# Kernel optimization log

Measured on AMD Instinct MI355X. Metric: run time of the kernel, lower is better.

## Reference

```python
import jax, jax.numpy as jnp
import numpy as np

H = 16
D_K = 64
HALF_WINDOW = 256  # window_size // 2 = 512 // 2


def setup_inputs() -> dict:
    key = jax.random.key(0)
    ks = jax.random.split(key, 9)
    B, S, D = 2, 2048, 1024
    scale = 0.02
    return {
        "x": jax.random.normal(ks[0], (B, S, D), dtype=jnp.float32),
        "Wq": jax.random.normal(ks[1], (D, D), dtype=jnp.float32) * scale,
        "bq": jax.random.normal(ks[2], (D,), dtype=jnp.float32) * scale,
        "Wk": jax.random.normal(ks[3], (D, D), dtype=jnp.float32) * scale,
        "bk": jax.random.normal(ks[4], (D,), dtype=jnp.float32) * scale,
        "Wv": jax.random.normal(ks[5], (D, D), dtype=jnp.float32) * scale,
        "bv": jax.random.normal(ks[6], (D,), dtype=jnp.float32) * scale,
        "Wo": jax.random.normal(ks[7], (D, D), dtype=jnp.float32) * scale,
        "bo": jax.random.normal(ks[8], (D,), dtype=jnp.float32) * scale,
    }


def reference(x, Wq, bq, Wk, bk, Wv, bv, Wo, bo):
    B, S, D = x.shape
    # projections -> [B, H, S, d_k]
    q = (x @ Wq + bq).reshape(B, S, H, D_K).transpose(0, 2, 1, 3)
    k = (x @ Wk + bk).reshape(B, S, H, D_K).transpose(0, 2, 1, 3)
    v = (x @ Wv + bv).reshape(B, S, H, D_K).transpose(0, 2, 1, 3)
    # dense scores, as in the original module
    scores = jnp.einsum("bhqd,bhkd->bhqk", q, k) / jnp.sqrt(jnp.float32(D_K))
    # sliding window band mask: 0 inside |i-j| <= half_window, -inf outside
    idx = jnp.arange(S)
    band = jnp.abs(idx[:, None] - idx[None, :]) <= HALF_WINDOW  # [S, S]
    window_mask = jnp.where(band, jnp.float32(0.0), -jnp.inf)
    scores = scores + window_mask[None, None, :, :]
    attn = jax.nn.softmax(scores, axis=-1)  # dropout is identity (p=0 / eval)
    out = jnp.einsum("bhqk,bhkd->bhqd", attn, v)  # [B, H, S, d_k]
    out = out.transpose(0, 2, 1, 3).reshape(B, S, D)
    return out @ Wo + bo
```

## Files before the change

### kernel.cpp

```cpp
#include <hip/hip_runtime.h>
#include <hip/hip_bf16.h>
#include <cstdint>
#include <cstddef>

using bf16 = __hip_bfloat16;
typedef __attribute__((ext_vector_type(8))) short bf16x8v;
typedef __attribute__((ext_vector_type(4))) float f32x4v;
typedef __attribute__((ext_vector_type(16))) float f32x16v;
typedef __attribute__((ext_vector_type(4))) int i32x4v;

__device__ __forceinline__ f32x4v mfma16x16x32(bf16x8v a, bf16x8v b, f32x4v c) {
  return __builtin_amdgcn_mfma_f32_16x16x32_bf16(a, b, c, 0, 0, 0);
}
__device__ __forceinline__ f32x16v mfma32x32x16(bf16x8v a, bf16x8v b, f32x16v c) {
  return __builtin_amdgcn_mfma_f32_32x32x16_bf16(a, b, c, 0, 0, 0);
}

__device__ __forceinline__ void lds_async16(const void* g, void* l) {
  __builtin_amdgcn_global_load_lds(
      (__attribute__((address_space(1))) void*)g,
      (__attribute__((address_space(3))) void*)l, 16, 0, 0);
}

__device__ __forceinline__ unsigned short f2bf_bits(float f) {
  union { bf16 h; unsigned short u; } cv;
  cv.h = __float2bfloat16(f);
  return cv.u;
}
__device__ __forceinline__ uint32_t pk_bf2(float a, float b) {
  return (uint32_t)f2bf_bits(a) | ((uint32_t)f2bf_bits(b) << 16);
}

#define QSC 0.18033688011111793f


__global__ void convert_x_k(const float* __restrict__ x, bf16* __restrict__ xb) {
  const int i = blockIdx.x * blockDim.x + threadIdx.x;
  const float4 v = reinterpret_cast<const float4*>(x)[i];
  ushort4 o;
  o.x = f2bf_bits(v.x); o.y = f2bf_bits(v.y);
  o.z = f2bf_bits(v.z); o.w = f2bf_bits(v.w);
  reinterpret_cast<ushort4*>(xb)[i] = o;
}

__global__ void transpose_w_k(const float* __restrict__ Wq, const float* __restrict__ Wk,
                              const float* __restrict__ Wv, const float* __restrict__ Wo,
                              bf16* __restrict__ wcat, bf16* __restrict__ wot) {
  __shared__ float tile[64][65];
  const int mat = blockIdx.z;
  const float* W = (mat == 0) ? Wq : (mat == 1) ? Wk : (mat == 2) ? Wv : Wo;
  bf16* dst = (mat < 3) ? (wcat + (size_t)mat * 1024 * 1024) : wot;
  const int n0 = blockIdx.x * 64, k0 = blockIdx.y * 64;
  const int tr = threadIdx.x >> 6, tc = threadIdx.x & 63;
#pragma unroll
  for (int it = 0; it < 16; ++it)
    tile[it * 4 + tr][tc] = W[(size_t)(k0 + it * 4 + tr) * 1024 + n0 + tc];
  __syncthreads();
#pragma unroll
  for (int it = 0; it < 16; ++it) {
    const int n = n0 + it * 4 + tr;
    dst[(size_t)n * 1024 + k0 + tc] = __float2bfloat16(tile[tc][it * 4 + tr]);
  }
}

__global__ void build_bias_k(const float* __restrict__ bq, const float* __restrict__ bk,
                             const float* __restrict__ bv, float* __restrict__ bcat) {
  const int i = blockIdx.x * 256 + threadIdx.x;
  if (i < 3072)
    bcat[i] = (i < 1024) ? bq[i] : (i < 2048) ? bk[i - 1024] : bv[i - 2048];
}

template <int EPI>
__global__ __launch_bounds__(256, 2) void gemm_k(
    const bf16* __restrict__ A, const bf16* __restrict__ Bt,
    const float* __restrict__ bias,
    bf16* __restrict__ qb, bf16* __restrict__ kb, bf16* __restrict__ vtb,
    float* __restrict__ outf)
{
  constexpr int K = 1024;
  __shared__ bf16 As[128 * 32];
  __shared__ bf16 Bs[128 * 32];
  const int t = threadIdx.x;
  const int lane = t & 63, w = t >> 6;
  const int g = lane >> 4, r = lane & 15;
  const int wr = w >> 1, wc = w & 1;
  const int m0 = blockIdx.x * 128, n0 = blockIdx.y * 128;

  const int srow = w * 16 + (lane >> 2);
  const int skoff = (lane & 3) * 8;
  const bf16* aSrc0 = A + (size_t)(m0 + srow) * K + skoff;
  const bf16* aSrc1 = aSrc0 + (size_t)64 * K;
  const bf16* bSrc0 = Bt + (size_t)(n0 + srow) * K + skoff;
  const bf16* bSrc1 = bSrc0 + (size_t)64 * K;
  bf16* aDst0 = As + w * 512;
  bf16* aDst1 = As + 2048 + w * 512;
  bf16* bDst0 = Bs + w * 512;
  bf16* bDst1 = Bs + 2048 + w * 512;

  f32x4v acc[4][4] = {};

  for (int kt = 0; kt < K; kt += 32) {
    lds_async16(aSrc0 + kt, aDst0);
    lds_async16(aSrc1 + kt, aDst1);
    lds_async16(bSrc0 + kt, bDst0);
    lds_async16(bSrc1 + kt, bDst1);
    __syncthreads();
    bf16x8v af[4], bfr[4];
#pragma unroll
    for (int m = 0; m < 4; ++m)
      af[m] = *reinterpret_cast<const bf16x8v*>(&As[(wr * 64 + m * 16 + r) * 32 + g * 8]);
#pragma unroll
    for (int n = 0; n < 4; ++n)
      bfr[n] = *reinterpret_cast<const bf16x8v*>(&Bs[(wc * 64 + n * 16 + r) * 32 + g * 8]);
#pragma unroll
    for (int m = 0; m < 4; ++m)
#pragma unroll
      for (int n = 0; n < 4; ++n)
        acc[m][n] = mfma16x16x32(af[m], bfr[n], acc[m][n]);
    __syncthreads();
  }

#pragma unroll
  for (int n = 0; n < 4; ++n) {
    const int gcol = n0 + wc * 64 + n * 16 + r;
    const float bv_ = bias[gcol];
    if (EPI == 0) {
      const int mat = gcol >> 10;
      const int d = gcol & 1023;
      const int hh = d >> 6, dk = d & 63;
#pragma unroll
      for (int m = 0; m < 4; ++m) {
#pragma unroll
        for (int v = 0; v < 4; ++v) {
          const int grow = m0 + wr * 64 + m * 16 + g * 4 + v;
          const int b = grow >> 11, s = grow & 2047;
          const float val = acc[m][n][v] + bv_;
          const size_t bh = (size_t)(b * 16 + hh);
          if (mat == 0)      qb[(bh * 2048 + s) * 64 + dk] = __float2bfloat16(val * QSC);
          else if (mat == 1) kb[(bh * 2048 + s) * 64 + dk] = __float2bfloat16(val);
          else               vtb[(bh * 64 + dk) * 2048 + s] = __float2bfloat16(val);
        }
      }
    } else {
#pragma unroll
      for (int m = 0; m < 4; ++m) {
#pragma unroll
        for (int v = 0; v < 4; ++v) {
          const int grow = m0 + wr * 64 + m * 16 + g * 4 + v;
          outf[(size_t)grow * 1024 + gcol] = acc[m][n][v] + bv_;
        }
      }
    }
  }
}

__global__ __launch_bounds__(64) void attn_k(
    const bf16* __restrict__ qb, const bf16* __restrict__ kb_,
    const bf16* __restrict__ vtb, bf16* __restrict__ aout)
{
  constexpr int S = 2048;
  const int lane = threadIdx.x & 63;
  const int hi = lane >> 5, l31 = lane & 31;
  const int d_ = blockIdx.x;
  const int xcd = d_ & 7, slot = d_ >> 3;
  const int bh_i = xcd * 4 + (slot >> 6);
  const int q0 = (slot & 63) * 32;
  const int b = bh_i >> 4, h = bh_i & 15;
  const size_t bh = (size_t)b * 16 + h;
  const bf16* qp = qb + bh * (size_t)(S * 64);
  const bf16* kp = kb_ + bh * (size_t)(S * 64);
  const bf16* vp = vtb + bh * (size_t)(64 * S);

  bf16x8v qf[4];
#pragma unroll
  for (int i = 0; i < 4; ++i)
    qf[i] = *reinterpret_cast<const bf16x8v*>(&qp[(size_t)(q0 + l31) * 64 + i * 16 + hi * 8]);

  f32x16v o0 = {}, o1 = {};
  float lrun = 0.f;

  const int jlo = (q0 >= 256) ? (q0 - 256) : 0;
  const int jend = (q0 + 256 <= S - 32) ? (q0 + 256) : (S - 32);
  const int nIter = ((jend - jlo) >> 5) + 1;

  auto LDK = [&](int j, bf16x8v* kf) {
    const bf16* p0 = kp + (size_t)(j + l31) * 64 + hi * 8;
#pragma unroll
    for (int i = 0; i < 4; ++i)
      kf[i] = *reinterpret_cast<const bf16x8v*>(p0 + i * 16);
  };
  auto LDV = [&](int j, bf16x8v* vf) {
#pragma unroll
    for (int db = 0; db < 2; ++db)
#pragma unroll
      for (int kk = 0; kk < 2; ++kk)
        vf[db * 2 + kk] = *reinterpret_cast<const bf16x8v*>(
            &vp[(size_t)(db * 32 + l31) * S + j + kk * 16 + hi * 8]);
  };

  auto STEP = [&](int idx, bf16x8v* kc, bf16x8v* vc, bf16x8v* kn, bf16x8v* vn) {
    const int j = jlo + idx * 32;
    if (idx + 1 < nIter) { LDK(j + 32, kn); LDV(j + 32, vn); }

    f32x16v s = {};
#pragma unroll
    for (int i = 0; i < 4; ++i) s = mfma32x32x16(kc[i], qf[i], s);

    float p[16];
    const bool needMask = ((q0 + 31 - j) > 256) || ((j + 31 - q0) > 256);
    if (needMask) {
      const int base = l31 - 4 * hi + (q0 - j) + 256;
#pragma unroll
      for (int t = 0; t < 4; ++t)
#pragma unroll
        for (int e = 0; e < 4; ++e) {
          const int kk_ = 8 * t + e;
          const float ev = __builtin_amdgcn_exp2f(s[4 * t + e]);
          p[4 * t + e] = ((unsigned)(base - kk_) <= 512u) ? ev : 0.f;
        }
    } else {
#pragma unroll
      for (int i = 0; i < 16; ++i) p[i] = __builtin_amdgcn_exp2f(s[i]);
    }
    lrun += (((p[0] + p[1]) + (p[2] + p[3])) + ((p[4] + p[5]) + (p[6] + p[7]))) +
            (((p[8] + p[9]) + (p[10] + p[11])) + ((p[12] + p[13]) + (p[14] + p[15])));

    uint32_t W00 = pk_bf2(p[0],  p[1]),  W01 = pk_bf2(p[2],  p[3]);
    uint32_t W10 = pk_bf2(p[4],  p[5]),  W11 = pk_bf2(p[6],  p[7]);
    uint32_t W20 = pk_bf2(p[8],  p[9]),  W21 = pk_bf2(p[10], p[11]);
    uint32_t W30 = pk_bf2(p[12], p[13]), W31 = pk_bf2(p[14], p[15]);
    asm volatile("v_permlane32_swap_b32 %0, %1" : "+v"(W00), "+v"(W10));
    asm volatile("v_permlane32_swap_b32 %0, %1" : "+v"(W01), "+v"(W11));
    asm volatile("v_permlane32_swap_b32 %0, %1" : "+v"(W20), "+v"(W30));
    asm volatile("v_permlane32_swap_b32 %0, %1" : "+v"(W21), "+v"(W31));
    union { i32x4v i; bf16x8v hv; } c0, c1;
    c0.i = (i32x4v){(int)W00, (int)W01, (int)W10, (int)W11};
    c1.i = (i32x4v){(int)W20, (int)W21, (int)W30, (int)W31};
    o0 = mfma32x32x16(vc[0], c0.hv, o0);
    o0 = mfma32x32x16(vc[1], c1.hv, o0);
    o1 = mfma32x32x16(vc[2], c0.hv, o1);
    o1 = mfma32x32x16(vc[3], c1.hv, o1);
  };

  bf16x8v ka[4], va[4], kn2[4], vn2[4];
  LDK(jlo, ka); LDV(jlo, va);
  int it = 0;
  while (it + 2 <= nIter) {
    STEP(it, ka, va, kn2, vn2);
    STEP(it + 1, kn2, vn2, ka, va);
    it += 2;
  }
  if (it < nIter) STEP(it, ka, va, kn2, vn2);

  lrun += __shfl_xor(lrun, 32);
  const float inv = 1.0f / lrun;

  const size_t ob = ((size_t)b * S + q0 + l31) * 1024 + h * 64 + hi * 4;
#pragma unroll
  for (int t = 0; t < 4; ++t) {
    uint2 u;
    u.x = pk_bf2(o0[4 * t] * inv, o0[4 * t + 1] * inv);
    u.y = pk_bf2(o0[4 * t + 2] * inv, o0[4 * t + 3] * inv);
    *reinterpret_cast<uint2*>(&aout[ob + 8 * t]) = u;
    uint2 v2;
    v2.x = pk_bf2(o1[4 * t] * inv, o1[4 * t + 1] * inv);
    v2.y = pk_bf2(o1[4 * t + 2] * inv, o1[4 * t + 3] * inv);
    *reinterpret_cast<uint2*>(&aout[ob + 32 + 8 * t]) = v2;
  }
}

extern "C" void kernel_launch(void* const* d_in, const int* in_sizes, int n_in,
                              void* d_out, int out_size, void* d_ws, size_t ws_size,
                              hipStream_t stream) {
  (void)in_sizes; (void)n_in; (void)out_size; (void)ws_size;
  const float* x  = (const float*)d_in[0];
  const float* Wq = (const float*)d_in[1];
  const float* bq = (const float*)d_in[2];
  const float* Wk = (const float*)d_in[3];
  const float* bk = (const float*)d_in[4];
  const float* Wv = (const float*)d_in[5];
  const float* bv = (const float*)d_in[6];
  const float* Wo = (const float*)d_in[7];
  const float* bo = (const float*)d_in[8];
  float* out = (float*)d_out;

  char* ws = (char*)d_ws;
  bf16*  xb    = (bf16*)(ws);
  bf16*  wcat  = (bf16*)(ws + 8388608);
  bf16*  wot   = (bf16*)(ws + 14680064);
  bf16*  qbuf  = (bf16*)(ws + 16777216);
  bf16*  kbuf  = (bf16*)(ws + 25165824);
  bf16*  vtbuf = (bf16*)(ws + 33554432);
  bf16*  aoutb = (bf16*)(ws + 41943040);
  float* bcat  = (float*)(ws + 50331648);

  convert_x_k<<<4096, 256, 0, stream>>>(x, xb);
  transpose_w_k<<<dim3(16, 16, 4), 256, 0, stream>>>(Wq, Wk, Wv, Wo, wcat, wot);
  build_bias_k<<<12, 256, 0, stream>>>(bq, bk, bv, bcat);

  gemm_k<0><<<dim3(32, 24), 256, 0, stream>>>(xb, wcat, bcat, qbuf, kbuf, vtbuf, nullptr);
  attn_k<<<2048, 64, 0, stream>>>(qbuf, kbuf, vtbuf, aoutb);
  gemm_k<1><<<dim3(32, 8), 256, 0, stream>>>(aoutb, wot, bo, nullptr, nullptr, nullptr, out);
}
```

Before: 112.4 us.

## Use 256x256-tile triple-buffered async GEMM for fused QKV projection

Replaces the 128x128 QKV projection GEMM with a dedicated kernel that uses 256x256 output tiles, 512 threads, and a three-stage LDS ring filled by async global-to-LDS loads with explicit vmcnt waits. This gives more operand reuse per tile and overlaps loads with MFMA work. It also remaps block IDs so consecutive tiles spread across XCDs. In exchange, 192 blocks is fewer than the CU count, which may leave compute units idle, and LDS use per block is larger.

```diff
diff --git a/kernel.cpp b/kernel.cpp
--- a/kernel.cpp
+++ b/kernel.cpp
@@ -70,12 +70,98 @@
     bcat[i] = (i < 1024) ? bq[i] : (i < 2048) ? bk[i - 1024] : bv[i - 2048];
 }
 
-template <int EPI>
+__global__ __launch_bounds__(512, 2) void gemm256_k(
+    const bf16* __restrict__ A, const bf16* __restrict__ Bt,
+    const float* __restrict__ bias,
+    bf16* __restrict__ qb, bf16* __restrict__ kb, bf16* __restrict__ vtb)
+{
+  constexpr int K = 1024;
+  constexpr int NTILE = 12;
+  __shared__ bf16 smem[3 * 16384];
+  const int t = threadIdx.x;
+  const int lane = t & 63, w = t >> 6;
+  const int g = lane >> 4, r = lane & 15;
+  const int wm = w >> 2, wn = w & 3;
+
+  const int d = blockIdx.x;
+  const int wg = (d & 7) * 24 + (d >> 3);
+  const int m0 = (wg / NTILE) * 256, n0 = (wg % NTILE) * 256;
+
+  const bf16* aS0 = A + (size_t)(m0 + (t >> 2)) * K + (t & 3) * 8;
+  const bf16* aS1 = aS0 + (size_t)128 * K;
+  const bf16* bS0 = Bt + (size_t)(n0 + (t >> 2)) * K + (t & 3) * 8;
+  const bf16* bS1 = bS0 + (size_t)128 * K;
+
+  f32x4v acc[8][4] = {};
+
+#define STAGE256(kt_, buf_)                                        \
+  {                                                                \
+    bf16* base_ = smem + (buf_) * 16384 + w * 512;                 \
+    const int off_ = (kt_) * 32;                                   \
+    lds_async16(aS0 + off_, base_);                                \
+    lds_async16(aS1 + off_, base_ + 4096);                         \
+    lds_async16(bS0 + off_, base_ + 8192);                         \
+    lds_async16(bS1 + off_, base_ + 12288);                        \
+  }
+
+  STAGE256(0, 0);
+  STAGE256(1, 1);
+
+  int cb = 0;
+  int sb = 2;
+  for (int kt = 0; kt < 32; ++kt) {
+    if (kt < 31) asm volatile("s_waitcnt vmcnt(4)" ::: "memory");
+    else         asm volatile("s_waitcnt vmcnt(0)" ::: "memory");
+    __builtin_amdgcn_s_barrier();
+    __builtin_amdgcn_sched_barrier(0);
+    if (kt < 30) STAGE256(kt + 2, sb);
+
+    const bf16* Ab = smem + cb * 16384 + (wm * 128 + r) * 32 + g * 8;
+    const bf16* Bb = smem + cb * 16384 + 8192 + (wn * 64 + r) * 32 + g * 8;
+    bf16x8v af[8], bfr[4];
+#pragma unroll
+    for (int m = 0; m < 8; ++m)
+      af[m] = *reinterpret_cast<const bf16x8v*>(Ab + m * 512);
+#pragma unroll
+    for (int n = 0; n < 4; ++n)
+      bfr[n] = *reinterpret_cast<const bf16x8v*>(Bb + n * 512);
+#pragma unroll
+    for (int m = 0; m < 8; ++m)
+#pragma unroll
+      for (int n = 0; n < 4; ++n)
+        acc[m][n] = mfma16x16x32(af[m], bfr[n], acc[m][n]);
+
+    cb = (cb == 2) ? 0 : cb + 1;
+    sb = (sb == 2) ? 0 : sb + 1;
+  }
+#undef STAGE256
+
+#pragma unroll
+  for (int n = 0; n < 4; ++n) {
+    const int gcol = n0 + wn * 64 + n * 16 + r;
+    const float bv_ = bias[gcol];
+    const int mat = gcol >> 10;
+    const int dcol = gcol & 1023;
+    const int hh = dcol >> 6, dk = dcol & 63;
+#pragma unroll
+    for (int m = 0; m < 8; ++m) {
+#pragma unroll
+      for (int v = 0; v < 4; ++v) {
+        const int grow = m0 + wm * 128 + m * 16 + g * 4 + v;
+        const int b = grow >> 11, s = grow & 2047;
+        const float val = acc[m][n][v] + bv_;
+        const size_t bh = (size_t)(b * 16 + hh);
+        if (mat == 0)      qb[(bh * 2048 + s) * 64 + dk] = __float2bfloat16(val * QSC);
+        else if (mat == 1) kb[(bh * 2048 + s) * 64 + dk] = __float2bfloat16(val);
+        else               vtb[(bh * 64 + dk) * 2048 + s] = __float2bfloat16(val);
+      }
+    }
+  }
+}
+
 __global__ __launch_bounds__(256, 2) void gemm_k(
     const bf16* __restrict__ A, const bf16* __restrict__ Bt,
-    const float* __restrict__ bias,
-    bf16* __restrict__ qb, bf16* __restrict__ kb, bf16* __restrict__ vtb,
-    float* __restrict__ outf)
+    const float* __restrict__ bias, float* __restrict__ outf)
 {
   constexpr int K = 1024;
   __shared__ bf16 As[128 * 32];
@@ -124,31 +210,12 @@
   for (int n = 0; n < 4; ++n) {
     const int gcol = n0 + wc * 64 + n * 16 + r;
     const float bv_ = bias[gcol];
-    if (EPI == 0) {
-      const int mat = gcol >> 10;
-      const int d = gcol & 1023;
-      const int hh = d >> 6, dk = d & 63;
-#pragma unroll
-      for (int m = 0; m < 4; ++m) {
-#pragma unroll
-        for (int v = 0; v < 4; ++v) {
-          const int grow = m0 + wr * 64 + m * 16 + g * 4 + v;
-          const int b = grow >> 11, s = grow & 2047;
-          const float val = acc[m][n][v] + bv_;
-          const size_t bh = (size_t)(b * 16 + hh);
-          if (mat == 0)      qb[(bh * 2048 + s) * 64 + dk] = __float2bfloat16(val * QSC);
-          else if (mat == 1) kb[(bh * 2048 + s) * 64 + dk] = __float2bfloat16(val);
-          else               vtb[(bh * 64 + dk) * 2048 + s] = __float2bfloat16(val);
-        }
-      }
-    } else {
-#pragma unroll
-      for (int m = 0; m < 4; ++m) {
-#pragma unroll
-        for (int v = 0; v < 4; ++v) {
-          const int grow = m0 + wr * 64 + m * 16 + g * 4 + v;
-          outf[(size_t)grow * 1024 + gcol] = acc[m][n][v] + bv_;
-        }
+#pragma unroll
+    for (int m = 0; m < 4; ++m) {
+#pragma unroll
+      for (int v = 0; v < 4; ++v) {
+        const int grow = m0 + wr * 64 + m * 16 + g * 4 + v;
+        outf[(size_t)grow * 1024 + gcol] = acc[m][n][v] + bv_;
       }
     }
   }
@@ -211,12 +278,12 @@
     if (needMask) {
       const int base = l31 - 4 * hi + (q0 - j) + 256;
 #pragma unroll
-      for (int t = 0; t < 4; ++t)
+      for (int tt = 0; tt < 4; ++tt)
 #pragma unroll
         for (int e = 0; e < 4; ++e) {
-          const int kk_ = 8 * t + e;
-          const float ev = __builtin_amdgcn_exp2f(s[4 * t + e]);
-          p[4 * t + e] = ((unsigned)(base - kk_) <= 512u) ? ev : 0.f;
+          const int kk_ = 8 * tt + e;
+          const float ev = __builtin_amdgcn_exp2f(s[4 * tt + e]);
+          p[4 * tt + e] = ((unsigned)(base - kk_) <= 512u) ? ev : 0.f;
         }
     } else {
 #pragma unroll
@@ -257,15 +324,15 @@
 
   const size_t ob = ((size_t)b * S + q0 + l31) * 1024 + h * 64 + hi * 4;
 #pragma unroll
-  for (int t = 0; t < 4; ++t) {
+  for (int tt = 0; tt < 4; ++tt) {
     uint2 u;
-    u.x = pk_bf2(o0[4 * t] * inv, o0[4 * t + 1] * inv);
-    u.y = pk_bf2(o0[4 * t + 2] * inv, o0[4 * t + 3] * inv);
-    *reinterpret_cast<uint2*>(&aout[ob + 8 * t]) = u;
+    u.x = pk_bf2(o0[4 * tt] * inv, o0[4 * tt + 1] * inv);
+    u.y = pk_bf2(o0[4 * tt + 2] * inv, o0[4 * tt + 3] * inv);
+    *reinterpret_cast<uint2*>(&aout[ob + 8 * tt]) = u;
     uint2 v2;
-    v2.x = pk_bf2(o1[4 * t] * inv, o1[4 * t + 1] * inv);
-    v2.y = pk_bf2(o1[4 * t + 2] * inv, o1[4 * t + 3] * inv);
-    *reinterpret_cast<uint2*>(&aout[ob + 32 + 8 * t]) = v2;
+    v2.x = pk_bf2(o1[4 * tt] * inv, o1[4 * tt + 1] * inv);
+    v2.y = pk_bf2(o1[4 * tt + 2] * inv, o1[4 * tt + 3] * inv);
+    *reinterpret_cast<uint2*>(&aout[ob + 32 + 8 * tt]) = v2;
   }
 }
 
@@ -298,7 +365,7 @@
   transpose_w_k<<<dim3(16, 16, 4), 256, 0, stream>>>(Wq, Wk, Wv, Wo, wcat, wot);
   build_bias_k<<<12, 256, 0, stream>>>(bq, bk, bv, bcat);
 
-  gemm_k<0><<<dim3(32, 24), 256, 0, stream>>>(xb, wcat, bcat, qbuf, kbuf, vtbuf, nullptr);
+  gemm256_k<<<192, 512, 0, stream>>>(xb, wcat, bcat, qbuf, kbuf, vtbuf);
   attn_k<<<2048, 64, 0, stream>>>(qbuf, kbuf, vtbuf, aoutb);
-  gemm_k<1><<<dim3(32, 8), 256, 0, stream>>>(aoutb, wot, bo, nullptr, nullptr, nullptr, out);
-}
+  gemm_k<<<dim3(32, 8), 256, 0, stream>>>(aoutb, wot, bo, out);
+}
```

Result: slower. 133.3 us (+18.7%).

## Deepen GEMM K-tile to 64 with XOR-swizzled LDS layout

Applied to the files above, without the earlier changes.

The projection GEMM now stages 64-wide K slices per iteration instead of 32, which halves the number of barrier pairs. Global-to-LDS loads use an XOR swizzle on the 16-byte chunk index so the fragment reads avoid LDS bank conflicts. The launch-bounds occupancy hint goes from 2 to 3 blocks, at the cost of doubled shared memory per block (32 KB) and tighter register pressure. Loop variables in the attention kernel are renamed to avoid shadowing.

```diff
diff --git a/kernel.cpp b/kernel.cpp
--- a/kernel.cpp
+++ b/kernel.cpp
@@ -71,52 +71,64 @@
 }
 
 template <int EPI>
-__global__ __launch_bounds__(256, 2) void gemm_k(
+__global__ __launch_bounds__(256, 3) void gemm_k(
     const bf16* __restrict__ A, const bf16* __restrict__ Bt,
     const float* __restrict__ bias,
     bf16* __restrict__ qb, bf16* __restrict__ kb, bf16* __restrict__ vtb,
     float* __restrict__ outf)
 {
   constexpr int K = 1024;
-  __shared__ bf16 As[128 * 32];
-  __shared__ bf16 Bs[128 * 32];
+  __shared__ bf16 As[128 * 64];
+  __shared__ bf16 Bs[128 * 64];
   const int t = threadIdx.x;
   const int lane = t & 63, w = t >> 6;
   const int g = lane >> 4, r = lane & 15;
   const int wr = w >> 1, wc = w & 1;
   const int m0 = blockIdx.x * 128, n0 = blockIdx.y * 128;
 
-  const int srow = w * 16 + (lane >> 2);
-  const int skoff = (lane & 3) * 8;
-  const bf16* aSrc0 = A + (size_t)(m0 + srow) * K + skoff;
-  const bf16* aSrc1 = aSrc0 + (size_t)64 * K;
-  const bf16* bSrc0 = Bt + (size_t)(n0 + srow) * K + skoff;
-  const bf16* bSrc1 = bSrc0 + (size_t)64 * K;
-  bf16* aDst0 = As + w * 512;
-  bf16* aDst1 = As + 2048 + w * 512;
-  bf16* bDst0 = Bs + w * 512;
-  bf16* bDst1 = Bs + 2048 + w * 512;
+  const bf16* aS[4];
+  const bf16* bS[4];
+  bf16* aD[4];
+  bf16* bD[4];
+#pragma unroll
+  for (int i = 0; i < 4; ++i) {
+    const int G = t + 256 * i;
+    const int row = G >> 3, gd = G & 7;
+    const int col = ((gd ^ (row & 7)) << 3);
+    aS[i] = A + (size_t)(m0 + row) * K + col;
+    bS[i] = Bt + (size_t)(n0 + row) * K + col;
+    aD[i] = As + w * 512 + i * 2048;
+    bD[i] = Bs + w * 512 + i * 2048;
+  }
 
   f32x4v acc[4][4] = {};
 
-  for (int kt = 0; kt < K; kt += 32) {
-    lds_async16(aSrc0 + kt, aDst0);
-    lds_async16(aSrc1 + kt, aDst1);
-    lds_async16(bSrc0 + kt, bDst0);
-    lds_async16(bSrc1 + kt, bDst1);
+  for (int kt = 0; kt < 16; ++kt) {
+    const int ko = kt * 64;
+#pragma unroll
+    for (int i = 0; i < 4; ++i) {
+      lds_async16(aS[i] + ko, aD[i]);
+      lds_async16(bS[i] + ko, bD[i]);
+    }
     __syncthreads();
-    bf16x8v af[4], bfr[4];
-#pragma unroll
-    for (int m = 0; m < 4; ++m)
-      af[m] = *reinterpret_cast<const bf16x8v*>(&As[(wr * 64 + m * 16 + r) * 32 + g * 8]);
-#pragma unroll
-    for (int n = 0; n < 4; ++n)
-      bfr[n] = *reinterpret_cast<const bf16x8v*>(&Bs[(wc * 64 + n * 16 + r) * 32 + g * 8]);
-#pragma unroll
-    for (int m = 0; m < 4; ++m)
-#pragma unroll
-      for (int n = 0; n < 4; ++n)
-        acc[m][n] = mfma16x16x32(af[m], bfr[n], acc[m][n]);
+
+#pragma unroll
+    for (int ks = 0; ks < 2; ++ks) {
+      const int csw = ((ks * 4 + g) ^ (r & 7)) << 4;
+      bf16x8v af[4];
+#pragma unroll
+      for (int m = 0; m < 4; ++m)
+        af[m] = *reinterpret_cast<const bf16x8v*>(
+            (const char*)As + (wr * 64 + m * 16 + r) * 128 + csw);
+#pragma unroll
+      for (int n = 0; n < 4; ++n) {
+        const bf16x8v bf_ = *reinterpret_cast<const bf16x8v*>(
+            (const char*)Bs + (wc * 64 + n * 16 + r) * 128 + csw);
+#pragma unroll
+        for (int m = 0; m < 4; ++m)
+          acc[m][n] = mfma16x16x32(af[m], bf_, acc[m][n]);
+      }
+    }
     __syncthreads();
   }
 
@@ -211,12 +223,12 @@
     if (needMask) {
       const int base = l31 - 4 * hi + (q0 - j) + 256;
 #pragma unroll
-      for (int t = 0; t < 4; ++t)
+      for (int tt = 0; tt < 4; ++tt)
 #pragma unroll
         for (int e = 0; e < 4; ++e) {
-          const int kk_ = 8 * t + e;
-          const float ev = __builtin_amdgcn_exp2f(s[4 * t + e]);
-          p[4 * t + e] = ((unsigned)(base - kk_) <= 512u) ? ev : 0.f;
+          const int kk_ = 8 * tt + e;
+          const float ev = __builtin_amdgcn_exp2f(s[4 * tt + e]);
+          p[4 * tt + e] = ((unsigned)(base - kk_) <= 512u) ? ev : 0.f;
         }
     } else {
 #pragma unroll
@@ -257,15 +269,15 @@
 
   const size_t ob = ((size_t)b * S + q0 + l31) * 1024 + h * 64 + hi * 4;
 #pragma unroll
-  for (int t = 0; t < 4; ++t) {
+  for (int tt = 0; tt < 4; ++tt) {
     uint2 u;
-    u.x = pk_bf2(o0[4 * t] * inv, o0[4 * t + 1] * inv);
-    u.y = pk_bf2(o0[4 * t + 2] * inv, o0[4 * t + 3] * inv);
-    *reinterpret_cast<uint2*>(&aout[ob + 8 * t]) = u;
+    u.x = pk_bf2(o0[4 * tt] * inv, o0[4 * tt + 1] * inv);
+    u.y = pk_bf2(o0[4 * tt + 2] * inv, o0[4 * tt + 3] * inv);
+    *reinterpret_cast<uint2*>(&aout[ob + 8 * tt]) = u;
     uint2 v2;
-    v2.x = pk_bf2(o1[4 * t] * inv, o1[4 * t + 1] * inv);
-    v2.y = pk_bf2(o1[4 * t + 2] * inv, o1[4 * t + 3] * inv);
-    *reinterpret_cast<uint2*>(&aout[ob + 32 + 8 * t]) = v2;
+    v2.x = pk_bf2(o1[4 * tt] * inv, o1[4 * tt + 1] * inv);
+    v2.y = pk_bf2(o1[4 * tt + 2] * inv, o1[4 * tt + 3] * inv);
+    *reinterpret_cast<uint2*>(&aout[ob + 32 + 8 * tt]) = v2;
   }
 }
 
```

After: 106.1 us. 1.06x faster.
